# Performance work log

Hardware: AMD Instinct MI355X
Metric: run time of the kernel (lower is better)

## Reference

```python
import jax, jax.numpy as jnp
import numpy as np

B, D, H = 32, 512, 1024


def setup_inputs() -> dict:
    key = jax.random.key(0)
    ks = jax.random.split(key, 9)
    x = jax.random.normal(ks[0], (B, D), dtype=jnp.float32)
    h0 = 0.1 * jax.random.normal(ks[1], (B, H), dtype=jnp.float32)
    c0 = 0.1 * jax.random.normal(ks[2], (B, H), dtype=jnp.float32)
    # Hebbian trace lives in [-1, 1] (clipped each step)
    Hebb0 = jax.random.uniform(ks[3], (B, H, H), dtype=jnp.float32, minval=-0.5, maxval=0.5)
    weight_h = jax.random.normal(ks[4], (H, 4 * H), dtype=jnp.float32) / np.sqrt(H)
    weight_x = jax.random.normal(ks[5], (D, 4 * H), dtype=jnp.float32) / np.sqrt(D)
    # bias init: zeros, forget-gate slice set to 1 (T_max=None path)
    bias = jnp.zeros((4 * H,), dtype=jnp.float32).at[:H].set(1.0)
    # alpha init is constant 0.01; add tiny noise for non-degenerate testing
    alpha = 0.01 + 0.001 * jax.random.normal(ks[6], (H, H), dtype=jnp.float32)
    eta = jnp.array([0.01], dtype=jnp.float32)
    return {"x": x, "h0": h0, "c0": c0, "Hebb0": Hebb0,
            "weight_h": weight_h, "weight_x": weight_x, "bias": bias,
            "alpha": alpha, "eta": eta}


def reference(x, h0, c0, Hebb0, weight_h, weight_x, bias, alpha, eta):
    Hs = h0.shape[1]
    # gates = h0 @ (weight_h + cat[0,0,0, alpha*Hebb]) + x @ weight_x + bias
    # The plastic term only affects the last (cell-gate) chunk; compute it
    # without materializing the (B,H,4H) dynamic weight tensor.
    gates = h0 @ weight_h + x @ weight_x + bias[None, :]
    plastic = jnp.einsum('bi,ih,bih->bh', h0, alpha, Hebb0)  # (B, H)
    f_g, i_g, o_g, g_g = jnp.split(gates, 4, axis=1)
    g_g = g_g + plastic  # cell gate gets the fast-weight contribution
    tanh_g = jnp.tanh(g_g)
    c1 = jax.nn.sigmoid(f_g) * c0 + jax.nn.sigmoid(i_g) * tanh_g
    h1 = jax.nn.sigmoid(o_g) * jnp.tanh(c1)
    # Hebbian outer-product update with clip (neuromodulation=None path)
    Hebb1 = jnp.clip(Hebb0 + eta[0] * jnp.einsum('bh,bi->bhi', h0, tanh_g), -1.0, 1.0)
    return h1, c1, Hebb1
```

## Files before the change

kernel.cpp:

```cpp
#include <hip/hip_runtime.h>
#include <math.h>

#define B 32
#define D 512
#define H 1024
#define G4 4096
#define PCH 32
#define GCH 12

__global__ __launch_bounds__(256) void k_plastic(
    const float* __restrict__ h0, const float* __restrict__ alpha,
    const float* __restrict__ hebb, float* __restrict__ pp) {
  int blk = blockIdx.x;
  int b = blk >> 5;
  int c = blk & (PCH - 1);
  int h4 = threadIdx.x * 4;
  int i0 = c * (H / PCH);
  const float* hb = hebb + (size_t)b * H * H;
  float4 acc = make_float4(0.f, 0.f, 0.f, 0.f);
  for (int i = i0; i < i0 + (H / PCH); ++i) {
    float hv = h0[b * H + i];
    float4 a = *(const float4*)(alpha + (size_t)i * H + h4);
    float4 e = *(const float4*)(hb + (size_t)i * H + h4);
    acc.x += hv * a.x * e.x;
    acc.y += hv * a.y * e.y;
    acc.z += hv * a.z * e.z;
    acc.w += hv * a.w * e.w;
  }
  *(float4*)(pp + ((size_t)c * B + b) * H + h4) = acc;
}

__global__ __launch_bounds__(256) void k_gates(
    const float* __restrict__ h0, const float* __restrict__ x,
    const float* __restrict__ wh, const float* __restrict__ wx,
    float* __restrict__ gp) {
  int j = blockIdx.x * 256 + threadIdx.x;
  int c = blockIdx.y;
  float acc[B];
#pragma unroll
  for (int b = 0; b < B; ++b) acc[b] = 0.f;
  if (c < 8) {
    int i0 = c * 128;
    for (int i = i0; i < i0 + 128; ++i) {
      float w = wh[(size_t)i * G4 + j];
#pragma unroll
      for (int b = 0; b < B; ++b) acc[b] += h0[b * H + i] * w;
    }
  } else {
    int i0 = (c - 8) * 128;
    for (int i = i0; i < i0 + 128; ++i) {
      float w = wx[(size_t)i * G4 + j];
#pragma unroll
      for (int b = 0; b < B; ++b) acc[b] += x[b * D + i] * w;
    }
  }
#pragma unroll
  for (int b = 0; b < B; ++b) gp[((size_t)c * B + b) * G4 + j] = acc[b];
}

__global__ __launch_bounds__(256) void k_combine(
    const float* __restrict__ gp, const float* __restrict__ pp,
    const float* __restrict__ bias, const float* __restrict__ c0,
    float* __restrict__ out, float* __restrict__ tg_out) {
  int t = blockIdx.x * 256 + threadIdx.x;
  int b = t >> 10;
  int h = t & (H - 1);
  float sf = bias[h], si = bias[H + h], so = bias[2 * H + h], sg = bias[3 * H + h];
#pragma unroll
  for (int c = 0; c < GCH; ++c) {
    const float* g = gp + ((size_t)c * B + b) * G4;
    sf += g[h];
    si += g[H + h];
    so += g[2 * H + h];
    sg += g[3 * H + h];
  }
#pragma unroll
  for (int c = 0; c < PCH; ++c) sg += pp[((size_t)c * B + b) * H + h];
  float fg = 1.f / (1.f + expf(-sf));
  float ig = 1.f / (1.f + expf(-si));
  float og = 1.f / (1.f + expf(-so));
  float tgv = tanhf(sg);
  float c1 = fg * c0[t] + ig * tgv;
  float h1 = og * tanhf(c1);
  out[t] = h1;
  out[B * H + t] = c1;
  tg_out[t] = tgv;
}

__global__ __launch_bounds__(256) void k_hebb(
    const float* __restrict__ hebb, const float* __restrict__ h0,
    const float* __restrict__ tg, const float* __restrict__ eta,
    float* __restrict__ out) {
  int blk = blockIdx.x;
  int b = blk >> 10;
  float s = eta[0] * h0[blk];
  int t4 = threadIdx.x * 4;
  float4 tv = *(const float4*)(tg + b * H + t4);
  const float* src = hebb + (size_t)blk * H + t4;
  float4 e = *(const float4*)src;
  float4 r;
  r.x = fminf(fmaxf(e.x + s * tv.x, -1.f), 1.f);
  r.y = fminf(fmaxf(e.y + s * tv.y, -1.f), 1.f);
  r.z = fminf(fmaxf(e.z + s * tv.z, -1.f), 1.f);
  r.w = fminf(fmaxf(e.w + s * tv.w, -1.f), 1.f);
  *(float4*)(out + (size_t)blk * H + t4) = r;
}

extern "C" void kernel_launch(void* const* d_in, const int* in_sizes, int n_in,
                              void* d_out, int out_size, void* d_ws, size_t ws_size,
                              hipStream_t stream) {
  const float* x     = (const float*)d_in[0];
  const float* h0    = (const float*)d_in[1];
  const float* c0    = (const float*)d_in[2];
  const float* hebb  = (const float*)d_in[3];
  const float* wh    = (const float*)d_in[4];
  const float* wx    = (const float*)d_in[5];
  const float* bias  = (const float*)d_in[6];
  const float* alpha = (const float*)d_in[7];
  const float* eta   = (const float*)d_in[8];
  float* out = (float*)d_out;
  float* ws  = (float*)d_ws;

  float* pp = ws;
  float* gp = pp + (size_t)PCH * B * H;
  float* tg = gp + (size_t)GCH * B * G4;

  k_plastic<<<B * PCH, 256, 0, stream>>>(h0, alpha, hebb, pp);
  k_gates<<<dim3(16, 12), 256, 0, stream>>>(h0, x, wh, wx, gp);
  k_combine<<<(B * H) / 256, 256, 0, stream>>>(gp, pp, bias, c0, out, tg);
  k_hebb<<<B * H, 256, 0, stream>>>(hebb, h0, tg, eta, out + 2 * B * H);
}
```

Baseline: 349.7 us.

## Fuse all LSTM stages into one cooperative persistent kernel with grid syncs

```diff
diff --git a/kernel.cpp b/kernel.cpp
--- a/kernel.cpp
+++ b/kernel.cpp
@@ -1,109 +1,126 @@
 #include <hip/hip_runtime.h>
+#include <hip/hip_cooperative_groups.h>
 #include <math.h>
 
 #define B 32
 #define D 512
 #define H 1024
 #define G4 4096
-#define PCH 32
+#define PCH 16
 #define GCH 12
+#define NBLK 704
 
-__global__ __launch_bounds__(256) void k_plastic(
-    const float* __restrict__ h0, const float* __restrict__ alpha,
-    const float* __restrict__ hebb, float* __restrict__ pp) {
-  int blk = blockIdx.x;
-  int b = blk >> 5;
-  int c = blk & (PCH - 1);
-  int h4 = threadIdx.x * 4;
-  int i0 = c * (H / PCH);
-  const float* hb = hebb + (size_t)b * H * H;
-  float4 acc = make_float4(0.f, 0.f, 0.f, 0.f);
-  for (int i = i0; i < i0 + (H / PCH); ++i) {
-    float hv = h0[b * H + i];
-    float4 a = *(const float4*)(alpha + (size_t)i * H + h4);
-    float4 e = *(const float4*)(hb + (size_t)i * H + h4);
-    acc.x += hv * a.x * e.x;
-    acc.y += hv * a.y * e.y;
-    acc.z += hv * a.z * e.z;
-    acc.w += hv * a.w * e.w;
+namespace cg = cooperative_groups;
+
+__global__ __launch_bounds__(256, 4) void k_fused(
+    const float* __restrict__ x, const float* __restrict__ h0,
+    const float* __restrict__ c0, const float* __restrict__ hebb,
+    const float* __restrict__ wh, const float* __restrict__ wx,
+    const float* __restrict__ bias, const float* __restrict__ alpha,
+    const float* __restrict__ eta, float* __restrict__ out,
+    float* __restrict__ pp, float* __restrict__ gp, float* __restrict__ tg) {
+  cg::grid_group grid = cg::this_grid();
+  const int blk = blockIdx.x;
+  const int tid = threadIdx.x;
+
+  if (blk < 192) {
+    const int c  = blk >> 4;
+    const int r  = blk & 15;
+    const int jb = r & 3;
+    const int b0 = (r >> 2) * 8;
+    const int j4 = jb * 1024 + tid * 4;
+    const float* W;
+    const float* in;
+    int i0, ld;
+    if (c < 8) { W = wh; in = h0; i0 = c * 128;       ld = H; }
+    else       { W = wx; in = x;  i0 = (c - 8) * 128; ld = D; }
+    float4 acc[8];
+#pragma unroll
+    for (int bb = 0; bb < 8; ++bb) acc[bb] = make_float4(0.f, 0.f, 0.f, 0.f);
+#pragma unroll 2
+    for (int i = i0; i < i0 + 128; ++i) {
+      float4 w = *(const float4*)(W + (size_t)i * G4 + j4);
+#pragma unroll
+      for (int bb = 0; bb < 8; ++bb) {
+        float hv = in[(b0 + bb) * ld + i];
+        acc[bb].x += hv * w.x;
+        acc[bb].y += hv * w.y;
+        acc[bb].z += hv * w.z;
+        acc[bb].w += hv * w.w;
+      }
+    }
+#pragma unroll
+    for (int bb = 0; bb < 8; ++bb)
+      *(float4*)(gp + ((size_t)c * B + b0 + bb) * G4 + j4) = acc[bb];
+  } else {
+    const int u = blk - 192;
+    const int b = u >> 4;
+    const int c = u & 15;
+    const int h4 = tid * 4;
+    const int i0 = c * 64;
+    const float* hb = hebb + (size_t)b * H * H;
+    float4 acc = make_float4(0.f, 0.f, 0.f, 0.f);
+#pragma unroll 4
+    for (int i = i0; i < i0 + 64; ++i) {
+      float hv = h0[b * H + i];
+      float4 a = *(const float4*)(alpha + (size_t)i * H + h4);
+      float4 e = *(const float4*)(hb + (size_t)i * H + h4);
+      acc.x += hv * a.x * e.x;
+      acc.y += hv * a.y * e.y;
+      acc.z += hv * a.z * e.z;
+      acc.w += hv * a.w * e.w;
+    }
+    *(float4*)(pp + ((size_t)c * B + b) * H + h4) = acc;
   }
-  *(float4*)(pp + ((size_t)c * B + b) * H + h4) = acc;
-}
 
-__global__ __launch_bounds__(256) void k_gates(
-    const float* __restrict__ h0, const float* __restrict__ x,
-    const float* __restrict__ wh, const float* __restrict__ wx,
-    float* __restrict__ gp) {
-  int j = blockIdx.x * 256 + threadIdx.x;
-  int c = blockIdx.y;
-  float acc[B];
+  grid.sync();
+
+  if (blk < 128) {
+    const int t = blk * 256 + tid;
+    const int b = t >> 10;
+    const int h = t & (H - 1);
+    float sf = bias[h], si = bias[H + h], so = bias[2 * H + h], sg = bias[3 * H + h];
 #pragma unroll
-  for (int b = 0; b < B; ++b) acc[b] = 0.f;
-  if (c < 8) {
-    int i0 = c * 128;
-    for (int i = i0; i < i0 + 128; ++i) {
-      float w = wh[(size_t)i * G4 + j];
+    for (int c = 0; c < GCH; ++c) {
+      const float* g = gp + ((size_t)c * B + b) * G4;
+      sf += g[h];
+      si += g[H + h];
+      so += g[2 * H + h];
+      sg += g[3 * H + h];
+    }
 #pragma unroll
-      for (int b = 0; b < B; ++b) acc[b] += h0[b * H + i] * w;
-    }
-  } else {
-    int i0 = (c - 8) * 128;
-    for (int i = i0; i < i0 + 128; ++i) {
-      float w = wx[(size_t)i * G4 + j];
-#pragma unroll
-      for (int b = 0; b < B; ++b) acc[b] += x[b * D + i] * w;
+    for (int c = 0; c < PCH; ++c) sg += pp[((size_t)c * B + b) * H + h];
+    float fg = 1.f / (1.f + expf(-sf));
+    float ig = 1.f / (1.f + expf(-si));
+    float og = 1.f / (1.f + expf(-so));
+    float tgv = tanhf(sg);
+    float c1 = fg * c0[t] + ig * tgv;
+    float h1 = og * tanhf(c1);
+    out[t] = h1;
+    out[B * H + t] = c1;
+    tg[t] = tgv;
+  }
+
+  grid.sync();
+
+  {
+    const float e = eta[0];
+    const int t4 = tid * 4;
+    float* out3 = out + 2 * B * H;
+#pragma unroll 2
+    for (int row = blk; row < B * H; row += NBLK) {
+      const int b = row >> 10;
+      const float s = e * h0[row];
+      float4 tv = *(const float4*)(tg + b * H + t4);
+      float4 v = *(const float4*)(hebb + (size_t)row * H + t4);
+      float4 rr;
+      rr.x = fminf(fmaxf(v.x + s * tv.x, -1.f), 1.f);
+      rr.y = fminf(fmaxf(v.y + s * tv.y, -1.f), 1.f);
+      rr.z = fminf(fmaxf(v.z + s * tv.z, -1.f), 1.f);
+      rr.w = fminf(fmaxf(v.w + s * tv.w, -1.f), 1.f);
+      *(float4*)(out3 + (size_t)row * H + t4) = rr;
     }
   }
-#pragma unroll
-  for (int b = 0; b < B; ++b) gp[((size_t)c * B + b) * G4 + j] = acc[b];
-}
-
-__global__ __launch_bounds__(256) void k_combine(
-    const float* __restrict__ gp, const float* __restrict__ pp,
-    const float* __restrict__ bias, const float* __restrict__ c0,
-    float* __restrict__ out, float* __restrict__ tg_out) {
-  int t = blockIdx.x * 256 + threadIdx.x;
-  int b = t >> 10;
-  int h = t & (H - 1);
-  float sf = bias[h], si = bias[H + h], so = bias[2 * H + h], sg = bias[3 * H + h];
-#pragma unroll
-  for (int c = 0; c < GCH; ++c) {
-    const float* g = gp + ((size_t)c * B + b) * G4;
-    sf += g[h];
-    si += g[H + h];
-    so += g[2 * H + h];
-    sg += g[3 * H + h];
-  }
-#pragma unroll
-  for (int c = 0; c < PCH; ++c) sg += pp[((size_t)c * B + b) * H + h];
-  float fg = 1.f / (1.f + expf(-sf));
-  float ig = 1.f / (1.f + expf(-si));
-  float og = 1.f / (1.f + expf(-so));
-  float tgv = tanhf(sg);
-  float c1 = fg * c0[t] + ig * tgv;
-  float h1 = og * tanhf(c1);
-  out[t] = h1;
-  out[B * H + t] = c1;
-  tg_out[t] = tgv;
-}
-
-__global__ __launch_bounds__(256) void k_hebb(
-    const float* __restrict__ hebb, const float* __restrict__ h0,
-    const float* __restrict__ tg, const float* __restrict__ eta,
-    float* __restrict__ out) {
-  int blk = blockIdx.x;
-  int b = blk >> 10;
-  float s = eta[0] * h0[blk];
-  int t4 = threadIdx.x * 4;
-  float4 tv = *(const float4*)(tg + b * H + t4);
-  const float* src = hebb + (size_t)blk * H + t4;
-  float4 e = *(const float4*)src;
-  float4 r;
-  r.x = fminf(fmaxf(e.x + s * tv.x, -1.f), 1.f);
-  r.y = fminf(fmaxf(e.y + s * tv.y, -1.f), 1.f);
-  r.z = fminf(fmaxf(e.z + s * tv.z, -1.f), 1.f);
-  r.w = fminf(fmaxf(e.w + s * tv.w, -1.f), 1.f);
-  *(float4*)(out + (size_t)blk * H + t4) = r;
 }
 
 extern "C" void kernel_launch(void* const* d_in, const int* in_sizes, int n_in,
@@ -125,8 +142,8 @@
   float* gp = pp + (size_t)PCH * B * H;
   float* tg = gp + (size_t)GCH * B * G4;
 
-  k_plastic<<<B * PCH, 256, 0, stream>>>(h0, alpha, hebb, pp);
-  k_gates<<<dim3(16, 12), 256, 0, stream>>>(h0, x, wh, wx, gp);
-  k_combine<<<(B * H) / 256, 256, 0, stream>>>(gp, pp, bias, c0, out, tg);
-  k_hebb<<<B * H, 256, 0, stream>>>(hebb, h0, tg, eta, out + 2 * B * H);
+  void* args[] = {(void*)&x, (void*)&h0, (void*)&c0, (void*)&hebb,
+                  (void*)&wh, (void*)&wx, (void*)&bias, (void*)&alpha,
+                  (void*)&eta, (void*)&out, (void*)&pp, (void*)&gp, (void*)&tg};
+  hipLaunchCooperativeKernel((void*)k_fused, dim3(NBLK), dim3(256), args, 0, stream);
 }
```

New measurement: 512.8 us. 1.47x slower.
